# Optimization experiments

Measured on AMD Instinct MI355X. Metric: run time of the kernel, lower is better.

## Reference

```python
import jax, jax.numpy as jnp
import numpy as np

B, C2D, C3D, H, W, N = 4, 64, 64, 256, 256, 16384
NEG_SLOPE = 0.1


def _conv1x1_lrelu(x, w, b):
    # 1x1 conv (no norm) + leaky_relu(0.1), per Conv2dNormRelu defaults
    y = jnp.einsum('bchw,oc->bohw', x, w) + b[None, :, None, None]
    return jax.nn.leaky_relu(y, NEG_SLOPE)


def _batch_gather(feat, idx):
    # feat: [B, C, N], idx: [B, P] -> [B, C, P]
    return jnp.take_along_axis(feat, idx[:, None, :], axis=2)


def setup_inputs() -> dict:
    key = jax.random.key(0)
    ks = jax.random.split(key, 14)
    f = jax.random.normal
    s = 0.05
    return {
        'xy': jax.random.uniform(ks[0], (B, 2, N), jnp.float32) * jnp.float32(W),
        'feat_2d': f(ks[1], (B, C2D, H, W), jnp.float32),
        'feat_3d': f(ks[2], (B, C3D, N), jnp.float32),
        'last_flow_2d': f(ks[3], (B, 2, H, W), jnp.float32),
        'last_flow_3d_to_2d': f(ks[4], (B, 2, N), jnp.float32),
        'nn_proj': jax.random.randint(ks[5], (B, H, W, 1), 0, N, jnp.int32),
        'w1': f(ks[6], (C3D, C3D + 5), jnp.float32) * s,
        'b1': f(ks[7], (C3D,), jnp.float32) * s,
        'w2': f(ks[8], (C3D, C3D), jnp.float32) * s,
        'b2': f(ks[9], (C3D,), jnp.float32) * s,
        'w3': f(ks[10], (C3D, C3D), jnp.float32) * s,
        'b3': f(ks[11], (C3D,), jnp.float32) * s,
        'wf': f(ks[12], (C2D, C2D + C3D), jnp.float32) * s,
        'bf': f(ks[13], (C2D,), jnp.float32) * s,
    }


def reference(xy, feat_2d, feat_3d, last_flow_2d, last_flow_3d_to_2d, nn_proj,
              w1, b1, w2, b2, w3, b3, wf, bf):
    b, _, h, w = feat_2d.shape
    # concat per-point flow onto 3D features: [B, C3D+2, N]
    feat_3d_aug = jnp.concatenate([feat_3d, last_flow_3d_to_2d], axis=1)

    idx = nn_proj[..., 0].reshape(b, h * w)  # nearest-neighbor point per pixel
    gathered = _batch_gather(feat_3d_aug, idx).reshape(b, -1, h, w)  # [B, C3D+2, H, W]
    xy_proj = _batch_gather(xy, idx).reshape(b, 2, h, w)             # [B, 2, H, W]

    # pixel-coordinate mesh grid: channel 0 = x (width), channel 1 = y (height)
    gy, gx = jnp.meshgrid(jnp.arange(h, dtype=xy.dtype), jnp.arange(w, dtype=xy.dtype), indexing='ij')
    grid = jnp.stack([gx, gy], axis=0)[None]  # [1, 2, H, W]
    offset = xy_proj - grid                    # [B, 2, H, W]

    # correlation between gathered 3D feats and 2D feats (channel mean)
    corr = jnp.mean(gathered[:, :C2D] * feat_2d, axis=1, keepdims=True)  # [B, 1, H, W]

    # last 2 channels are the projected flow; subtract detached last_flow_2d
    flow_ch = gathered[:, -2:] - jax.lax.stop_gradient(last_flow_2d)
    x = jnp.concatenate([corr, offset, gathered[:, :-2], flow_ch], axis=1)  # [B, C3D+5, H, W]

    x = _conv1x1_lrelu(x, w1, b1)
    x = _conv1x1_lrelu(x, w2, b2)
    x = _conv1x1_lrelu(x, w3, b3)
    out = _conv1x1_lrelu(jnp.concatenate([x, feat_2d], axis=1), wf, bf)  # [B, C2D, H, W]
    return out
```

## Files before the change

kernel.cpp:

```cpp
#include <hip/hip_runtime.h>

#define BB 4
#define CH 64
#define HW 65536
#define NN 16384
#define NT 128
#define F2PITCH 72
#define W1OFS 0
#define W2OFS 4096
#define W3OFS 8192
#define WFOFS 12288
#define W2L 0
#define W3L 4096
#define WFL 8192
#define FWS_BYTE 46080
#define PTAB_BYTE 49152
#define PT_ROW 160
#define WS_NEED ((size_t)PTAB_BYTE + (size_t)BB * NN * PT_ROW)

typedef __attribute__((ext_vector_type(8))) short short8;
typedef __attribute__((ext_vector_type(4))) float f32x4;

union frag_u { unsigned short u[8]; short8 v; };
union frag2_u { unsigned short u[8]; unsigned int d[4]; short8 v; };
union bfrag { uint4 qv; short8 v; unsigned short u[8]; };
union half_u { uint4 q[2]; unsigned short u[16]; };

static __device__ __forceinline__ unsigned short f2bf(float x) {
    unsigned int u = __float_as_uint(x);
    return (unsigned short)((u + 0x7fffu + ((u >> 16) & 1u)) >> 16);
}
static __device__ __forceinline__ float bf2f(unsigned short h) {
    return __uint_as_float(((unsigned int)h) << 16);
}
static __device__ __forceinline__ unsigned int cvtpk(float a, float b) {
    unsigned int r;
    asm("v_cvt_pk_bf16_f32 %0, %1, %2" : "=v"(r) : "v"(a), "v"(b));
    return r;
}

__global__ __launch_bounds__(256) void prep(
    const float* __restrict__ xy, const float* __restrict__ f3d,
    const float* __restrict__ lf3d,
    const float* __restrict__ w1, const float* __restrict__ b1,
    const float* __restrict__ w2, const float* __restrict__ b2,
    const float* __restrict__ w3, const float* __restrict__ b3,
    const float* __restrict__ wf, const float* __restrict__ bf,
    unsigned short* __restrict__ wpk, float* __restrict__ fws,
    char* __restrict__ pt)
{
    const int t = threadIdx.x;
    const int bx = blockIdx.x;
    if (bx >= NN / 64) {
        if (blockIdx.y != 0) return;
        const int blk = bx - NN / 64;
        if (blk == 0) {
            for (int i = t; i < 64 * 64; i += 256) {
                const int m = i >> 6, k = i & 63;
                wpk[W1OFS + i] = f2bf(w1[m * 69 + 3 + k]);
            }
        } else if (blk == 1) {
            for (int i = t; i < 64 * 64; i += 256) wpk[W2OFS + i] = f2bf(w2[i]);
        } else if (blk == 2) {
            for (int i = t; i < 64 * 64; i += 256) wpk[W3OFS + i] = f2bf(w3[i]);
        } else if (blk == 3) {
            for (int i = t; i < 64 * 128; i += 256) wpk[WFOFS + i] = f2bf(wf[i]);
        } else if (t < 64) {
            fws[t]       = b1[t];
            fws[64 + t]  = b2[t];
            fws[128 + t] = b3[t];
            fws[192 + t] = bf[t];
            fws[256 + t] = w1[t * 69 + 1];
            fws[320 + t] = w1[t * 69 + 2];
            fws[384 + t] = w1[t * 69 + 0];
            fws[448 + t] = w1[t * 69 + 67];
            fws[512 + t] = w1[t * 69 + 68];
        }
        return;
    }
    const int cq = t >> 6;
    const int l = t & 63;
    const int gn = bx * 64 + l;
    const int b = blockIdx.y;
    half_u r;
#pragma unroll
    for (int i = 0; i < 16; i++)
        r.u[i] = f2bf(f3d[(size_t)(b * CH + cq * 16 + i) * NN + gn]);
    char* row = pt + ((size_t)b * NN + gn) * PT_ROW;
    uint4* rq = (uint4*)row;
    rq[2 * cq] = r.q[0];
    rq[2 * cq + 1] = r.q[1];
    if (cq == 0) {
        float4 e;
        e.x = xy[(size_t)(b * 2 + 0) * NN + gn];
        e.y = xy[(size_t)(b * 2 + 1) * NN + gn];
        e.z = lf3d[(size_t)(b * 2 + 0) * NN + gn];
        e.w = lf3d[(size_t)(b * 2 + 1) * NN + gn];
        *(float4*)(row + 144) = e;
    }
}

static __device__ __forceinline__ void wstage(
    const unsigned short* __restrict__ wpk, unsigned short* wl, int tid)
{
#pragma unroll 1
    for (int m = 0; m < 2; m++) {
        const char* g = (const char*)(wpk + W2OFS + m * 4096);
        char* l = (char*)(wl + m * 4096);
        for (int i = tid; i < 512; i += 256) {
            const int row = i >> 3, cb = (i & 7) * 16;
            const uint4 v = *(const uint4*)(g + row * 128 + cb);
            *(uint4*)(l + row * 128 + (cb ^ ((row & 7) << 4))) = v;
        }
    }
    {
        const char* g = (const char*)(wpk + WFOFS);
        char* l = (char*)(wl + WFL);
        for (int i = tid; i < 1024; i += 256) {
            const int row = i >> 4, cb = (i & 15) * 16;
            const uint4 v = *(const uint4*)(g + row * 256 + cb);
            *(uint4*)(l + row * 256 + (cb ^ ((row & 7) << 4))) = v;
        }
    }
}

struct pref_t {
    float4 fv[8];
    bfrag g4[2][2];
    float4 e;
    float lfx, lfy;
};

static __device__ __forceinline__ void tile_load(
    pref_t& P, const float* __restrict__ feat2d, const float* __restrict__ lf2d,
    const char* __restrict__ ptab, int b, int p_base, int w, int lane,
    int i0, int i1)
{
    const int ci = lane >> 3, qd = lane & 7;
    const int px0 = 32 * w + qd * 4;
#pragma unroll
    for (int cc = 0; cc < 8; cc++)
        P.fv[cc] = *(const float4*)(feat2d + (size_t)(b * CH + ci * 8 + cc) * HW + p_base + px0);
    const int q = lane >> 4;
    const uint4* r0 = (const uint4*)(ptab + ((size_t)b * NN + i0) * PT_ROW);
    const uint4* r1 = (const uint4*)(ptab + ((size_t)b * NN + i1) * PT_ROW);
#pragma unroll
    for (int kt = 0; kt < 2; kt++) {
        P.g4[0][kt].qv = r0[kt * 4 + (q & 3)];
        P.g4[1][kt].qv = r1[kt * 4 + (q & 3)];
    }
    if (lane < 32) {
        const char* re = (const char*)(lane >= 16 ? r1 : r0);
        P.e = *(const float4*)(re + 144);
        P.lfx = lf2d[(size_t)(b * 2 + 0) * HW + p_base + 32 * w + lane];
        P.lfy = lf2d[(size_t)(b * 2 + 1) * HW + p_base + 32 * w + lane];
    }
}

static __device__ __forceinline__ void tile_stage(
    const pref_t& P, unsigned short* F2, int w, int lane)
{
    const int ci = lane >> 3, qd = lane & 7;
    const int px0 = 32 * w + qd * 4;
#pragma unroll
    for (int px = 0; px < 4; px++) {
        frag2_u fr;
#pragma unroll
        for (int cc = 0; cc < 4; cc++)
            fr.d[cc] = cvtpk(((const float*)&P.fv[2 * cc])[px], ((const float*)&P.fv[2 * cc + 1])[px]);
        *(short8*)&F2[(px0 + px) * F2PITCH + ci * 8] = fr.v;
    }
}

static __device__ __forceinline__ void tile_corr(
    const pref_t& P, const unsigned short* F2, float* offsS, float* auxS,
    int p_base, int w, int lane, int q, int ln)
{
    float ca0 = 0.f, ca1 = 0.f;
#pragma unroll
    for (int kt = 0; kt < 2; kt++) {
        frag_u f0, f1;
        f0.v = *(const short8*)&F2[(32 * w + ln) * F2PITCH + kt * 32 + q * 8];
        f1.v = *(const short8*)&F2[(32 * w + 16 + ln) * F2PITCH + kt * 32 + q * 8];
#pragma unroll
        for (int j = 0; j < 8; j++) {
            ca0 += bf2f(f0.u[j]) * bf2f(P.g4[0][kt].u[j]);
            ca1 += bf2f(f1.u[j]) * bf2f(P.g4[1][kt].u[j]);
        }
    }
    ca0 += __shfl_xor(ca0, 16); ca0 += __shfl_xor(ca0, 32);
    ca1 += __shfl_xor(ca1, 16); ca1 += __shfl_xor(ca1, 32);
    if (lane < 32) {
        const int n = 32 * w + lane;
        const int p = p_base + n;
        offsS[n] = P.e.x - (float)(p & 255);
        offsS[NT + n] = P.e.y - (float)(p >> 8);
        auxS[n] = (lane >= 16 ? ca1 : ca0) * (1.0f / 64.0f);
        auxS[NT + n] = P.e.z - P.lfx;
        auxS[2 * NT + n] = P.e.w - P.lfy;
    }
}

template<int RB>
static __device__ __forceinline__ void layer_reg(
    const unsigned short* wrow,
    const unsigned int pkH[4][2][2], const unsigned int pkL[4][2][2],
    int srcA, int srcB, int qh, int ln, int q, int swz, f32x4 acc[4][2])
{
#pragma unroll
    for (int kt = 0; kt < 2; kt++) {
        const int kb = (kt * 32 + q * 8) * 2;
        short8 A[4];
#pragma unroll
        for (int mi = 0; mi < 4; mi++)
            A[mi] = *(const short8*)((const char*)wrow + (mi * 16 + ln) * RB + (kb ^ swz));
#pragma unroll
        for (int ni = 0; ni < 2; ni++) {
            frag2_u bh, bl;
#pragma unroll
            for (int p = 0; p < 4; p++) {
                const int src = (p >> 1) ? srcB : srcA;
                const unsigned h0 = (unsigned)__builtin_amdgcn_ds_bpermute(src, (int)pkH[kt * 2 + 0][ni][p & 1]);
                const unsigned h1 = (unsigned)__builtin_amdgcn_ds_bpermute(src, (int)pkH[kt * 2 + 1][ni][p & 1]);
                bh.d[p] = qh ? h1 : h0;
                const unsigned l0 = (unsigned)__builtin_amdgcn_ds_bpermute(src, (int)pkL[kt * 2 + 0][ni][p & 1]);
                const unsigned l1 = (unsigned)__builtin_amdgcn_ds_bpermute(src, (int)pkL[kt * 2 + 1][ni][p & 1]);
                bl.d[p] = qh ? l1 : l0;
            }
            __builtin_amdgcn_s_setprio(1);
#pragma unroll
            for (int mi = 0; mi < 4; mi++) {
                acc[mi][ni] = __builtin_amdgcn_mfma_f32_16x16x32_bf16(A[mi], bh.v, acc[mi][ni], 0, 0, 0);
                acc[mi][ni] = __builtin_amdgcn_mfma_f32_16x16x32_bf16(A[mi], bl.v, acc[mi][ni], 0, 0, 0);
            }
            __builtin_amdgcn_s_setprio(0);
        }
    }
}

static __device__ __forceinline__ void zero_acc(f32x4 acc[4][2]) {
#pragma unroll
    for (int mi = 0; mi < 4; mi++)
#pragma unroll
        for (int ni = 0; ni < 2; ni++)
#pragma unroll
            for (int r = 0; r < 4; r++) acc[mi][ni][r] = 0.f;
}

static __device__ __forceinline__ void epi_pack(
    f32x4 acc[4][2], const float* __restrict__ fws, int bofs, bool off_fix,
    const float* offsp, const float* auxp,
    unsigned int pkH[4][2][2], unsigned int pkL[4][2][2],
    int w, int ln, int q)
{
#pragma unroll
    for (int mi = 0; mi < 4; mi++) {
        const float4 bias = *(const float4*)(fws + bofs + mi * 16 + q * 4);
        float4 wox = bias, woy = bias, wco = bias, wfx = bias, wfy = bias;
        if (off_fix) {
            wox = *(const float4*)(fws + 256 + mi * 16 + q * 4);
            woy = *(const float4*)(fws + 320 + mi * 16 + q * 4);
            wco = *(const float4*)(fws + 384 + mi * 16 + q * 4);
            wfx = *(const float4*)(fws + 448 + mi * 16 + q * 4);
            wfy = *(const float4*)(fws + 512 + mi * 16 + q * 4);
        }
#pragma unroll
        for (int ni = 0; ni < 2; ni++) {
            const int nr = 32 * w + ni * 16 + ln;
            float ox = 0.f, oy = 0.f, co = 0.f, fx = 0.f, fy = 0.f;
            if (off_fix) {
                ox = offsp[nr]; oy = offsp[NT + nr];
                co = auxp[nr];  fx = auxp[NT + nr]; fy = auxp[2 * NT + nr];
            }
            float av[4];
#pragma unroll
            for (int r = 0; r < 4; r++) {
                float a = acc[mi][ni][r] + ((const float*)&bias)[r];
                if (off_fix) {
                    a += ((const float*)&wox)[r] * ox + ((const float*)&woy)[r] * oy;
                    a += ((const float*)&wco)[r] * co;
                    a += ((const float*)&wfx)[r] * fx + ((const float*)&wfy)[r] * fy;
                }
                av[r] = fmaxf(a, 0.1f * a);
            }
#pragma unroll
            for (int t = 0; t < 2; t++) {
                const unsigned hh = cvtpk(av[2 * t], av[2 * t + 1]);
                const float l0 = av[2 * t]     - __uint_as_float(hh << 16);
                const float l1 = av[2 * t + 1] - __uint_as_float(hh & 0xffff0000u);
                pkH[mi][ni][t] = hh;
                pkL[mi][ni][t] = cvtpk(l0, l1);
            }
        }
    }
}

__global__ __launch_bounds__(256, 3) void fuse(
    const float* __restrict__ feat2d, const float* __restrict__ lf2d,
    const int* __restrict__ nn,
    const unsigned short* __restrict__ wpk, const float* __restrict__ fws,
    const char* __restrict__ ptab,
    float* __restrict__ out)
{
    __shared__ unsigned short F2[NT * F2PITCH];
    __shared__ unsigned short Wl[16384];
    __shared__ float offsS[2 * NT];
    __shared__ float auxS[3 * NT];

    const int tid = threadIdx.x;
    const int w = tid >> 6, lane = tid & 63;
    const int q = lane >> 4, ln = lane & 15;
    const int b = blockIdx.y;
    const int p0 = blockIdx.x * NT;

    const int srcA = (((lane >> 4) & 1) * 32 + ln) * 4;
    const int srcB = srcA + 64;
    const int qh = q >> 1;
    const int swz = (ln & 7) << 4;

    const int i0 = nn[(size_t)b * HW + p0 + 32 * w + ln];
    const int i1 = nn[(size_t)b * HW + p0 + 32 * w + 16 + ln];

    pref_t P;
    tile_load(P, feat2d, lf2d, ptab, b, p0, w, lane, i0, i1);
    wstage(wpk, Wl, tid);
    __syncthreads();

    short8 A1[2][4];
#pragma unroll
    for (int kt = 0; kt < 2; kt++)
#pragma unroll
        for (int mi = 0; mi < 4; mi++)
            A1[kt][mi] = *(const short8*)(wpk + W1OFS + (mi * 16 + ln) * 64 + kt * 32 + q * 8);

    tile_stage(P, F2, w, lane);
    tile_corr(P, F2, offsS, auxS, p0, w, lane, q, ln);

    unsigned int pkH[4][2][2], pkL[4][2][2];
    f32x4 acc[4][2];
    zero_acc(acc);
#pragma unroll
    for (int kt = 0; kt < 2; kt++) {
#pragma unroll
        for (int ni = 0; ni < 2; ni++) {
            __builtin_amdgcn_s_setprio(1);
#pragma unroll
            for (int mi = 0; mi < 4; mi++)
                acc[mi][ni] = __builtin_amdgcn_mfma_f32_16x16x32_bf16(A1[kt][mi], P.g4[ni][kt].v, acc[mi][ni], 0, 0, 0);
            __builtin_amdgcn_s_setprio(0);
        }
    }
    epi_pack(acc, fws, 0, true, offsS, auxS, pkH, pkL, w, ln, q);
#pragma unroll 1
    for (int l = 0; l < 2; l++) {
        zero_acc(acc);
        layer_reg<128>(Wl + W2L + (l << 12), pkH, pkL, srcA, srcB, qh, ln, q, swz, acc);
        epi_pack(acc, fws, 64 + (l << 6), false, offsS, auxS, pkH, pkL, w, ln, q);
    }
    zero_acc(acc);
    layer_reg<256>(Wl + WFL, pkH, pkL, srcA, srcB, qh, ln, q, swz, acc);
#pragma unroll
    for (int kt = 2; kt < 4; kt++) {
        const int kb = (kt * 32 + q * 8) * 2;
        short8 A[4];
#pragma unroll
        for (int mi = 0; mi < 4; mi++)
            A[mi] = *(const short8*)((const char*)(Wl + WFL) + (mi * 16 + ln) * 256 + (kb ^ swz));
#pragma unroll
        for (int ni = 0; ni < 2; ni++) {
            const int nr = 32 * w + ni * 16 + ln;
            frag_u fh;
            fh.v = *(const short8*)&F2[nr * F2PITCH + (kt - 2) * 32 + q * 8];
            __builtin_amdgcn_s_setprio(1);
#pragma unroll
            for (int mi = 0; mi < 4; mi++)
                acc[mi][ni] = __builtin_amdgcn_mfma_f32_16x16x32_bf16(A[mi], fh.v, acc[mi][ni], 0, 0, 0);
            __builtin_amdgcn_s_setprio(0);
        }
    }
#pragma unroll
    for (int mi = 0; mi < 4; mi++) {
        const float4 bias = *(const float4*)(fws + 192 + mi * 16 + q * 4);
#pragma unroll
        for (int ni = 0; ni < 2; ni++) {
#pragma unroll
            for (int r = 0; r < 4; r++) {
                float a = acc[mi][ni][r] + ((const float*)&bias)[r];
                a = fmaxf(a, 0.1f * a);
                const int m = mi * 16 + q * 4 + r;
                out[(size_t)(b * CH + m) * HW + p0 + 32 * w + ni * 16 + ln] = a;
            }
        }
    }
}

__global__ __launch_bounds__(256) void fuse_slow(
    const float* __restrict__ feat2d, const float* __restrict__ lf2d,
    const float* __restrict__ xy, const float* __restrict__ feat3d,
    const float* __restrict__ lf3d, const int* __restrict__ nn,
    const float* __restrict__ w1, const float* __restrict__ b1,
    const float* __restrict__ w2, const float* __restrict__ b2,
    const float* __restrict__ w3, const float* __restrict__ b3,
    const float* __restrict__ wf, const float* __restrict__ bfv,
    float* __restrict__ out)
{
    const int p = blockIdx.x * 256 + threadIdx.x;
    const int b = blockIdx.y;
    const int idx = nn[(size_t)b * HW + p];
    const float* f3 = feat3d + (size_t)b * CH * NN + idx;
    float g[CH];
#pragma unroll
    for (int c = 0; c < CH; c++) g[c] = f3[(size_t)c * NN];
    const float fl3x = lf3d[(size_t)(b * 2 + 0) * NN + idx];
    const float fl3y = lf3d[(size_t)(b * 2 + 1) * NN + idx];
    const float xyx = xy[(size_t)(b * 2 + 0) * NN + idx];
    const float xyy = xy[(size_t)(b * 2 + 1) * NN + idx];
    const float* f2p = feat2d + (size_t)b * CH * HW + p;
    float corr = 0.f;
#pragma unroll
    for (int c = 0; c < CH; c++) corr += f2p[(size_t)c * HW] * g[c];
    corr *= (1.f / 64.f);
    float xin[69];
    xin[0] = corr;
    xin[1] = xyx - (float)(p & 255);
    xin[2] = xyy - (float)(p >> 8);
#pragma unroll
    for (int c = 0; c < CH; c++) xin[3 + c] = g[c];
    xin[67] = fl3x - lf2d[(size_t)(b * 2 + 0) * HW + p];
    xin[68] = fl3y - lf2d[(size_t)(b * 2 + 1) * HW + p];
    float x1[64], x2[64], x3[64], accv[64];
#pragma unroll
    for (int o = 0; o < 64; o++) {
        float a = b1[o];
#pragma unroll
        for (int k = 0; k < 69; k++) a += w1[o * 69 + k] * xin[k];
        x1[o] = (a >= 0.f) ? a : 0.1f * a;
    }
#pragma unroll
    for (int o = 0; o < 64; o++) {
        float a = b2[o];
#pragma unroll
        for (int k = 0; k < 64; k++) a += w2[o * 64 + k] * x1[k];
        x2[o] = (a >= 0.f) ? a : 0.1f * a;
    }
#pragma unroll
    for (int o = 0; o < 64; o++) {
        float a = b3[o];
#pragma unroll
        for (int k = 0; k < 64; k++) a += w3[o * 64 + k] * x2[k];
        x3[o] = (a >= 0.f) ? a : 0.1f * a;
    }
#pragma unroll
    for (int o = 0; o < 64; o++) {
        float a = bfv[o];
#pragma unroll
        for (int k = 0; k < 64; k++) a += wf[o * 128 + k] * x3[k];
        accv[o] = a;
    }
#pragma unroll
    for (int k = 0; k < 64; k++) {
        const float f = f2p[(size_t)k * HW];
#pragma unroll
        for (int o = 0; o < 64; o++) accv[o] += wf[o * 128 + 64 + k] * f;
    }
#pragma unroll
    for (int o = 0; o < 64; o++) {
        float a = accv[o];
        a = (a >= 0.f) ? a : 0.1f * a;
        out[(size_t)(b * CH + o) * HW + p] = a;
    }
}

extern "C" void kernel_launch(void* const* d_in, const int* in_sizes, int n_in,
                              void* d_out, int out_size, void* d_ws, size_t ws_size,
                              hipStream_t stream)
{
    const float* xy   = (const float*)d_in[0];
    const float* f2d  = (const float*)d_in[1];
    const float* f3d  = (const float*)d_in[2];
    const float* lf2d = (const float*)d_in[3];
    const float* lf3d = (const float*)d_in[4];
    const int*   nn   = (const int*)d_in[5];
    const float* w1 = (const float*)d_in[6];
    const float* b1 = (const float*)d_in[7];
    const float* w2 = (const float*)d_in[8];
    const float* b2 = (const float*)d_in[9];
    const float* w3 = (const float*)d_in[10];
    const float* b3 = (const float*)d_in[11];
    const float* wf = (const float*)d_in[12];
    const float* bf = (const float*)d_in[13];

    if (ws_size >= WS_NEED) {
        unsigned short* wpk = (unsigned short*)d_ws;
        float* fws = (float*)((char*)d_ws + FWS_BYTE);
        char* pt = (char*)d_ws + PTAB_BYTE;
        prep<<<dim3(NN / 64 + 5, BB), 256, 0, stream>>>(xy, f3d, lf3d,
                                                        w1, b1, w2, b2, w3, b3, wf, bf,
                                                        wpk, fws, pt);
        fuse<<<dim3(HW / NT, BB), 256, 0, stream>>>(f2d, lf2d, nn, wpk, fws, pt, (float*)d_out);
    } else {
        fuse_slow<<<dim3(HW / 256, BB), 256, 0, stream>>>(f2d, lf2d, xy, f3d, lf3d, nn,
                                                          w1, b1, w2, b2, w3, b3, wf, bf,
                                                          (float*)d_out);
    }
}
```

Baseline: 201.1 us.

## Process two pixel tiles per block to amortize weight staging and interleave MFMAs

Each block now handles two 128-pixel tiles (A and B) instead of one, which halves the grid. Weight fragments loaded from LDS are reused across both tiles, and the two independent MFMA chains are interleaved to hide latency. The cost is doubled register and LDS use per block, with launch bounds lowered from 3 to 2 blocks per SM. That lowers occupancy and could cause spills.

```diff
diff --git a/kernel.cpp b/kernel.cpp
--- a/kernel.cpp
+++ b/kernel.cpp
@@ -5,13 +5,13 @@
 #define HW 65536
 #define NN 16384
 #define NT 128
+#define TW 256
 #define F2PITCH 72
 #define W1OFS 0
 #define W2OFS 4096
 #define W3OFS 8192
 #define WFOFS 12288
 #define W2L 0
-#define W3L 4096
 #define WFL 8192
 #define FWS_BYTE 46080
 #define PTAB_BYTE 49152
@@ -202,10 +202,12 @@
 }
 
 template<int RB>
-static __device__ __forceinline__ void layer_reg(
+static __device__ __forceinline__ void layer_reg2(
     const unsigned short* wrow,
-    const unsigned int pkH[4][2][2], const unsigned int pkL[4][2][2],
-    int srcA, int srcB, int qh, int ln, int q, int swz, f32x4 acc[4][2])
+    const unsigned int pkHA[4][2][2], const unsigned int pkLA[4][2][2],
+    const unsigned int pkHB[4][2][2], const unsigned int pkLB[4][2][2],
+    int bpa, int bpb, int qh, int ln, int q, int swz,
+    f32x4 accA[4][2], f32x4 accB[4][2])
 {
 #pragma unroll
     for (int kt = 0; kt < 2; kt++) {
@@ -216,22 +218,30 @@
             A[mi] = *(const short8*)((const char*)wrow + (mi * 16 + ln) * RB + (kb ^ swz));
 #pragma unroll
         for (int ni = 0; ni < 2; ni++) {
-            frag2_u bh, bl;
+            frag2_u bhA, blA, bhB, blB;
 #pragma unroll
             for (int p = 0; p < 4; p++) {
-                const int src = (p >> 1) ? srcB : srcA;
-                const unsigned h0 = (unsigned)__builtin_amdgcn_ds_bpermute(src, (int)pkH[kt * 2 + 0][ni][p & 1]);
-                const unsigned h1 = (unsigned)__builtin_amdgcn_ds_bpermute(src, (int)pkH[kt * 2 + 1][ni][p & 1]);
-                bh.d[p] = qh ? h1 : h0;
-                const unsigned l0 = (unsigned)__builtin_amdgcn_ds_bpermute(src, (int)pkL[kt * 2 + 0][ni][p & 1]);
-                const unsigned l1 = (unsigned)__builtin_amdgcn_ds_bpermute(src, (int)pkL[kt * 2 + 1][ni][p & 1]);
-                bl.d[p] = qh ? l1 : l0;
+                const int src = (p >> 1) ? bpb : bpa;
+                unsigned h0 = (unsigned)__builtin_amdgcn_ds_bpermute(src, (int)pkHA[kt * 2 + 0][ni][p & 1]);
+                unsigned h1 = (unsigned)__builtin_amdgcn_ds_bpermute(src, (int)pkHA[kt * 2 + 1][ni][p & 1]);
+                bhA.d[p] = qh ? h1 : h0;
+                unsigned l0 = (unsigned)__builtin_amdgcn_ds_bpermute(src, (int)pkLA[kt * 2 + 0][ni][p & 1]);
+                unsigned l1 = (unsigned)__builtin_amdgcn_ds_bpermute(src, (int)pkLA[kt * 2 + 1][ni][p & 1]);
+                blA.d[p] = qh ? l1 : l0;
+                h0 = (unsigned)__builtin_amdgcn_ds_bpermute(src, (int)pkHB[kt * 2 + 0][ni][p & 1]);
+                h1 = (unsigned)__builtin_amdgcn_ds_bpermute(src, (int)pkHB[kt * 2 + 1][ni][p & 1]);
+                bhB.d[p] = qh ? h1 : h0;
+                l0 = (unsigned)__builtin_amdgcn_ds_bpermute(src, (int)pkLB[kt * 2 + 0][ni][p & 1]);
+                l1 = (unsigned)__builtin_amdgcn_ds_bpermute(src, (int)pkLB[kt * 2 + 1][ni][p & 1]);
+                blB.d[p] = qh ? l1 : l0;
             }
             __builtin_amdgcn_s_setprio(1);
 #pragma unroll
             for (int mi = 0; mi < 4; mi++) {
-                acc[mi][ni] = __builtin_amdgcn_mfma_f32_16x16x32_bf16(A[mi], bh.v, acc[mi][ni], 0, 0, 0);
-                acc[mi][ni] = __builtin_amdgcn_mfma_f32_16x16x32_bf16(A[mi], bl.v, acc[mi][ni], 0, 0, 0);
+                accA[mi][ni] = __builtin_amdgcn_mfma_f32_16x16x32_bf16(A[mi], bhA.v, accA[mi][ni], 0, 0, 0);
+                accA[mi][ni] = __builtin_amdgcn_mfma_f32_16x16x32_bf16(A[mi], blA.v, accA[mi][ni], 0, 0, 0);
+                accB[mi][ni] = __builtin_amdgcn_mfma_f32_16x16x32_bf16(A[mi], bhB.v, accB[mi][ni], 0, 0, 0);
+                accB[mi][ni] = __builtin_amdgcn_mfma_f32_16x16x32_bf16(A[mi], blB.v, accB[mi][ni], 0, 0, 0);
             }
             __builtin_amdgcn_s_setprio(0);
         }
@@ -295,34 +305,61 @@
     }
 }
 
-__global__ __launch_bounds__(256, 3) void fuse(
+static __device__ __forceinline__ void out_store(
+    f32x4 acc[4][2], const float* __restrict__ fws, float* __restrict__ out,
+    int b, int p_base, int w, int ln, int q)
+{
+#pragma unroll
+    for (int mi = 0; mi < 4; mi++) {
+        const float4 bias = *(const float4*)(fws + 192 + mi * 16 + q * 4);
+#pragma unroll
+        for (int ni = 0; ni < 2; ni++) {
+#pragma unroll
+            for (int r = 0; r < 4; r++) {
+                float a = acc[mi][ni][r] + ((const float*)&bias)[r];
+                a = fmaxf(a, 0.1f * a);
+                const int m = mi * 16 + q * 4 + r;
+                out[(size_t)(b * CH + m) * HW + p_base + 32 * w + ni * 16 + ln] = a;
+            }
+        }
+    }
+}
+
+__global__ __launch_bounds__(256, 2) void fuse(
     const float* __restrict__ feat2d, const float* __restrict__ lf2d,
     const int* __restrict__ nn,
     const unsigned short* __restrict__ wpk, const float* __restrict__ fws,
     const char* __restrict__ ptab,
     float* __restrict__ out)
 {
-    __shared__ unsigned short F2[NT * F2PITCH];
+    __shared__ unsigned short F2A[NT * F2PITCH];
+    __shared__ unsigned short F2B[NT * F2PITCH];
     __shared__ unsigned short Wl[16384];
-    __shared__ float offsS[2 * NT];
-    __shared__ float auxS[3 * NT];
+    __shared__ float offsA[2 * NT];
+    __shared__ float auxA[3 * NT];
+    __shared__ float offsB[2 * NT];
+    __shared__ float auxB[3 * NT];
 
     const int tid = threadIdx.x;
     const int w = tid >> 6, lane = tid & 63;
     const int q = lane >> 4, ln = lane & 15;
     const int b = blockIdx.y;
-    const int p0 = blockIdx.x * NT;
-
-    const int srcA = (((lane >> 4) & 1) * 32 + ln) * 4;
-    const int srcB = srcA + 64;
+    const int p0 = blockIdx.x * TW;
+    const int pA = p0, pB = p0 + NT;
+
+    const int bpa = (((lane >> 4) & 1) * 32 + ln) * 4;
+    const int bpb = bpa + 64;
     const int qh = q >> 1;
     const int swz = (ln & 7) << 4;
 
-    const int i0 = nn[(size_t)b * HW + p0 + 32 * w + ln];
-    const int i1 = nn[(size_t)b * HW + p0 + 32 * w + 16 + ln];
-
-    pref_t P;
-    tile_load(P, feat2d, lf2d, ptab, b, p0, w, lane, i0, i1);
+    const int i0A = nn[(size_t)b * HW + pA + 32 * w + ln];
+    const int i1A = nn[(size_t)b * HW + pA + 32 * w + 16 + ln];
+    const int i0B = nn[(size_t)b * HW + pB + 32 * w + ln];
+    const int i1B = nn[(size_t)b * HW + pB + 32 * w + 16 + ln];
+
+    pref_t PA, PB;
+    tile_load(PA, feat2d, lf2d, ptab, b, pA, w, lane, i0A, i1A);
+    tile_load(PB, feat2d, lf2d, ptab, b, pB, w, lane, i0B, i1B);
     wstage(wpk, Wl, tid);
     __syncthreads();
 
@@ -333,32 +370,39 @@
         for (int mi = 0; mi < 4; mi++)
             A1[kt][mi] = *(const short8*)(wpk + W1OFS + (mi * 16 + ln) * 64 + kt * 32 + q * 8);
 
-    tile_stage(P, F2, w, lane);
-    tile_corr(P, F2, offsS, auxS, p0, w, lane, q, ln);
-
-    unsigned int pkH[4][2][2], pkL[4][2][2];
-    f32x4 acc[4][2];
-    zero_acc(acc);
+    tile_stage(PA, F2A, w, lane);
+    tile_stage(PB, F2B, w, lane);
+    tile_corr(PA, F2A, offsA, auxA, pA, w, lane, q, ln);
+    tile_corr(PB, F2B, offsB, auxB, pB, w, lane, q, ln);
+
+    unsigned int pkHA[4][2][2], pkLA[4][2][2], pkHB[4][2][2], pkLB[4][2][2];
+    f32x4 accA[4][2], accB[4][2];
+    zero_acc(accA); zero_acc(accB);
 #pragma unroll
     for (int kt = 0; kt < 2; kt++) {
 #pragma unroll
         for (int ni = 0; ni < 2; ni++) {
             __builtin_amdgcn_s_setprio(1);
 #pragma unroll
-            for (int mi = 0; mi < 4; mi++)
-                acc[mi][ni] = __builtin_amdgcn_mfma_f32_16x16x32_bf16(A1[kt][mi], P.g4[ni][kt].v, acc[mi][ni], 0, 0, 0);
+            for (int mi = 0; mi < 4; mi++) {
+                accA[mi][ni] = __builtin_amdgcn_mfma_f32_16x16x32_bf16(A1[kt][mi], PA.g4[ni][kt].v, accA[mi][ni], 0, 0, 0);
+                accB[mi][ni] = __builtin_amdgcn_mfma_f32_16x16x32_bf16(A1[kt][mi], PB.g4[ni][kt].v, accB[mi][ni], 0, 0, 0);
+            }
             __builtin_amdgcn_s_setprio(0);
         }
     }
-    epi_pack(acc, fws, 0, true, offsS, auxS, pkH, pkL, w, ln, q);
+    epi_pack(accA, fws, 0, true, offsA, auxA, pkHA, pkLA, w, ln, q);
+    epi_pack(accB, fws, 0, true, offsB, auxB, pkHB, pkLB, w, ln, q);
 #pragma unroll 1
     for (int l = 0; l < 2; l++) {
-        zero_acc(acc);
-        layer_reg<128>(Wl + W2L + (l << 12), pkH, pkL, srcA, srcB, qh, ln, q, swz, acc);
-        epi_pack(acc, fws, 64 + (l << 6), false, offsS, auxS, pkH, pkL, w, ln, q);
-    }
-    zero_acc(acc);
-    layer_reg<256>(Wl + WFL, pkH, pkL, srcA, srcB, qh, ln, q, swz, acc);
+        zero_acc(accA); zero_acc(accB);
+        layer_reg2<128>(Wl + W2L + (l << 12), pkHA, pkLA, pkHB, pkLB,
+                        bpa, bpb, qh, ln, q, swz, accA, accB);
+        epi_pack(accA, fws, 64 + (l << 6), false, offsA, auxA, pkHA, pkLA, w, ln, q);
+        epi_pack(accB, fws, 64 + (l << 6), false, offsB, auxB, pkHB, pkLB, w, ln, q);
+    }
+    zero_acc(accA); zero_acc(accB);
+    layer_reg2<256>(Wl + WFL, pkHA, pkLA, pkHB, pkLB, bpa, bpb, qh, ln, q, swz, accA, accB);
 #pragma unroll
     for (int kt = 2; kt < 4; kt++) {
         const int kb = (kt * 32 + q * 8) * 2;
@@ -369,29 +413,20 @@
 #pragma unroll
         for (int ni = 0; ni < 2; ni++) {
             const int nr = 32 * w + ni * 16 + ln;
-            frag_u fh;
-            fh.v = *(const short8*)&F2[nr * F2PITCH + (kt - 2) * 32 + q * 8];
+            frag_u fhA, fhB;
+            fhA.v = *(const short8*)&F2A[nr * F2PITCH + (kt - 2) * 32 + q * 8];
+            fhB.v = *(const short8*)&F2B[nr * F2PITCH + (kt - 2) * 32 + q * 8];
             __builtin_amdgcn_s_setprio(1);
 #pragma unroll
-            for (int mi = 0; mi < 4; mi++)
-                acc[mi][ni] = __builtin_amdgcn_mfma_f32_16x16x32_bf16(A[mi], fh.v, acc[mi][ni], 0, 0, 0);
+            for (int mi = 0; mi < 4; mi++) {
+                accA[mi][ni] = __builtin_amdgcn_mfma_f32_16x16x32_bf16(A[mi], fhA.v, accA[mi][ni], 0, 0, 0);
+                accB[mi][ni] = __builtin_amdgcn_mfma_f32_16x16x32_bf16(A[mi], fhB.v, accB[mi][ni], 0, 0, 0);
+            }
             __builtin_amdgcn_s_setprio(0);
         }
     }
-#pragma unroll
-    for (int mi = 0; mi < 4; mi++) {
-        const float4 bias = *(const float4*)(fws + 192 + mi * 16 + q * 4);
-#pragma unroll
-        for (int ni = 0; ni < 2; ni++) {
-#pragma unroll
-            for (int r = 0; r < 4; r++) {
-                float a = acc[mi][ni][r] + ((const float*)&bias)[r];
-                a = fmaxf(a, 0.1f * a);
-                const int m = mi * 16 + q * 4 + r;
-                out[(size_t)(b * CH + m) * HW + p0 + 32 * w + ni * 16 + ln] = a;
-            }
-        }
-    }
+    out_store(accA, fws, out, b, pA, w, ln, q);
+    out_store(accB, fws, out, b, pB, w, ln, q);
 }
 
 __global__ __launch_bounds__(256) void fuse_slow(
@@ -497,7 +532,7 @@
         prep<<<dim3(NN / 64 + 5, BB), 256, 0, stream>>>(xy, f3d, lf3d,
                                                         w1, b1, w2, b2, w3, b3, wf, bf,
                                                         wpk, fws, pt);
-        fuse<<<dim3(HW / NT, BB), 256, 0, stream>>>(f2d, lf2d, nn, wpk, fws, pt, (float*)d_out);
+        fuse<<<dim3(HW / TW, BB), 256, 0, stream>>>(f2d, lf2d, nn, wpk, fws, pt, (float*)d_out);
     } else {
         fuse_slow<<<dim3(HW / 256, BB), 256, 0, stream>>>(f2d, lf2d, xy, f3d, lf3d, nn,
                                                           w1, b1, w2, b2, w3, b3, wf, bf,
```

Result: no change. 201.2 us (+0.1%).
